# Kernel optimization log

Hardware: AMD Instinct MI355X
Metric: run time of the kernel (lower is better)

Reference implementation:

```python
import jax, jax.numpy as jnp
import numpy as np

B, D, O = 512, 256, 256
H = [512, 1024, 1024]

def _linear_params(key, fan_in, fan_out):
    kw, kb = jax.random.split(key)
    bound = 1.0 / np.sqrt(fan_in)
    W = jax.random.uniform(kw, (fan_out, fan_in), jnp.float32, -bound, bound)
    b = jax.random.uniform(kb, (fan_out,), jnp.float32, -bound, bound)
    return W, b

def setup_inputs() -> dict:
    key = jax.random.key(0)
    ks = jax.random.split(key, 7)
    input_values = jax.random.normal(ks[0], (B, D), jnp.float32)
    nan_flag = jax.random.uniform(ks[1], (B, D), jnp.float32)
    W_in, b_in = _linear_params(ks[2], D, H[0])          # input_layer: nan_flag_dim -> H[0]
    W_h1, b_h1 = _linear_params(ks[3], H[0], H[1])        # hidden layer 1
    W_h2, b_h2 = _linear_params(ks[4], H[1], H[2])        # hidden layer 2
    W_d, b_d = _linear_params(ks[5], H[2], D * O)         # output_branch_dense
    W_b, b_b = _linear_params(ks[6], H[2], O)             # output_branch_bias
    return {"input_values": input_values, "nan_flag": nan_flag, "training": False,
            "W_in": W_in, "b_in": b_in, "W_h1": W_h1, "b_h1": b_h1,
            "W_h2": W_h2, "b_h2": b_h2, "W_d": W_d, "b_d": b_d,
            "W_b": W_b, "b_b": b_b}

def reference(input_values, nan_flag, training, W_in, b_in, W_h1, b_h1, W_h2, b_h2, W_d, b_d, W_b, b_b):
    # training=False: dropout is identity, sample_missing branch skipped (default False)
    x = jax.nn.relu(nan_flag @ W_in.T + b_in)
    x = jax.nn.relu(x @ W_h1.T + b_h1)
    x = jax.nn.relu(x @ W_h2.T + b_h2)
    # per-sample compensation weights [B, D, O] and bias [B, O]
    comp_w = (x @ W_d.T + b_d).reshape(B, D, O)
    comp_b = x @ W_b.T + b_b
    # baddbmm: [B,1,D] @ [B,D,O] + [B,1,O] -> squeeze -> [B,O]
    out = comp_b + jnp.einsum('bd,bdo->bo', input_values, comp_w)
    return out
```

## Files before the change

kernel.cpp:

```cpp
#include <hip/hip_runtime.h>

#define B_  512
#define D_  256
#define O_  256
#define H2_ 1024

typedef __attribute__((ext_vector_type(4))) float  f32x4;
typedef __attribute__((ext_vector_type(8))) short  short8;
typedef __attribute__((ext_vector_type(4))) short  short4v;
typedef unsigned short ushort_t;

union S8u  { short4v v; unsigned u[2]; };
union S16u { short8  v; unsigned u[4]; };

__device__ __forceinline__ unsigned f32_bf16(float x) {
  unsigned u = __builtin_bit_cast(unsigned, x);
  return (u + 0x7fffu + ((u >> 16) & 1u)) >> 16;
}
__device__ __forceinline__ unsigned cvt_pk_bf16(float a, float b) {
  return f32_bf16(a) | (f32_bf16(b) << 16);
}

__device__ __forceinline__ void gload_lds16(const void* g, void* l) {
  __builtin_amdgcn_global_load_lds(
      (const __attribute__((address_space(1))) unsigned*)g,
      (__attribute__((address_space(3))) unsigned*)l, 16, 0, 0);
}

template <int RELU>
__global__ __launch_bounds__(256)
void gemm_bt64(const float* __restrict__ A, const float* __restrict__ Bm,
               const float* __restrict__ bias, float* __restrict__ C,
               int M, int N, int K) {
  __shared__ __align__(16) short As[64][72];
  __shared__ __align__(16) short Bs[64][72];
  const int t    = threadIdx.x;
  const int m0   = blockIdx.y * 64;
  const int n0   = blockIdx.x * 64;
  const int f4c  = t & 15;
  const int rg   = t >> 4;
  const int lane = t & 63;
  const int w    = t >> 6;
  const int wm   = (w & 1) * 32;
  const int wn   = (w >> 1) * 32;
  const int lr   = lane & 15;
  const int lq   = lane >> 4;

  f32x4 acc[2][2];
  #pragma unroll
  for (int i = 0; i < 2; ++i)
    #pragma unroll
    for (int j = 0; j < 2; ++j) acc[i][j] = f32x4{0.f, 0.f, 0.f, 0.f};

  for (int k0 = 0; k0 < K; k0 += 64) {
    #pragma unroll
    for (int j = 0; j < 4; ++j) {
      int r = rg + 16 * j;
      f32x4 av = *(const f32x4*)(A  + (size_t)(m0 + r) * K + k0 + f4c * 4);
      f32x4 bv = *(const f32x4*)(Bm + (size_t)(n0 + r) * K + k0 + f4c * 4);
      S8u sa; sa.u[0] = cvt_pk_bf16(av.x, av.y); sa.u[1] = cvt_pk_bf16(av.z, av.w);
      S8u sb; sb.u[0] = cvt_pk_bf16(bv.x, bv.y); sb.u[1] = cvt_pk_bf16(bv.z, bv.w);
      *(short4v*)&As[r][f4c * 4] = sa.v;
      *(short4v*)&Bs[r][f4c * 4] = sb.v;
    }
    __syncthreads();
    #pragma unroll
    for (int ks = 0; ks < 2; ++ks) {
      short8 a0 = *(const short8*)&As[wm + lr     ][ks * 32 + lq * 8];
      short8 a1 = *(const short8*)&As[wm + 16 + lr][ks * 32 + lq * 8];
      short8 b0 = *(const short8*)&Bs[wn + lr     ][ks * 32 + lq * 8];
      short8 b1 = *(const short8*)&Bs[wn + 16 + lr][ks * 32 + lq * 8];
      acc[0][0] = __builtin_amdgcn_mfma_f32_16x16x32_bf16(a0, b0, acc[0][0], 0, 0, 0);
      acc[0][1] = __builtin_amdgcn_mfma_f32_16x16x32_bf16(a0, b1, acc[0][1], 0, 0, 0);
      acc[1][0] = __builtin_amdgcn_mfma_f32_16x16x32_bf16(a1, b0, acc[1][0], 0, 0, 0);
      acc[1][1] = __builtin_amdgcn_mfma_f32_16x16x32_bf16(a1, b1, acc[1][1], 0, 0, 0);
    }
    __syncthreads();
  }
  #pragma unroll
  for (int mi = 0; mi < 2; ++mi)
    #pragma unroll
    for (int ni = 0; ni < 2; ++ni)
      #pragma unroll
      for (int r = 0; r < 4; ++r) {
        int row = m0 + wm + mi * 16 + lq * 4 + r;
        int col = n0 + wn + ni * 16 + lr;
        float v = acc[mi][ni][r] + bias[col];
        if (RELU) v = fmaxf(v, 0.f);
        C[(size_t)row * N + col] = v;
      }
}

__global__ __launch_bounds__(256)
void bias_d_kernel(const float* __restrict__ inp, const float* __restrict__ b_d,
                   float* __restrict__ out) {
  const int b = blockIdx.x;
  const int o = threadIdx.x;
  const float* ir = inp + (size_t)b * D_;
  float s = 0.f;
  for (int d = 0; d < D_; ++d)
    s += ir[d] * b_d[(size_t)d * O_ + o];
  out[(size_t)b * O_ + o] += s;
}

__global__ __launch_bounds__(256)
void cvt_f32_bf16(const float* __restrict__ in, ushort_t* __restrict__ out, int n8) {
  for (size_t i = (size_t)blockIdx.x * 256 + threadIdx.x; i < (size_t)n8;
       i += (size_t)gridDim.x * 256) {
    const float* p = in + i * 8;
    f32x4 v0 = *(const f32x4*)p;
    f32x4 v1 = *(const f32x4*)(p + 4);
    S16u s;
    s.u[0] = cvt_pk_bf16(v0.x, v0.y);
    s.u[1] = cvt_pk_bf16(v0.z, v0.w);
    s.u[2] = cvt_pk_bf16(v1.x, v1.y);
    s.u[3] = cvt_pk_bf16(v1.z, v1.w);
    *(short8*)(out + i * 8) = s.v;
  }
}

__global__ __launch_bounds__(512, 2)
void stage_b4(const ushort_t* __restrict__ x2b, const float* __restrict__ inp,
              const float* __restrict__ Wd, float* __restrict__ out) {
  __shared__ __align__(16) ushort_t As[2][256 * 32];
  __shared__ __align__(16) ushort_t Bs[2][256 * 32];
  const int t    = threadIdx.x;
  const int lin  = blockIdx.x + 8 * blockIdx.y;
  const int mt   = lin >> 8;
  const int nb   = lin & 255;
  const int d0   = (nb >> 4) * 16;
  const int og   = (nb & 15) * 16;
  const int bm   = mt * 256;
  const int lane = t & 63;
  const int w    = t >> 6;
  const int wm   = (w >> 1) * 64;
  const int wn   = (w & 1) * 128;
  const int lr   = lane & 15;
  const int lq   = lane >> 4;

  const int arow = lane >> 2;
  const int aswz = (lane & 3) ^ ((lane >> 3) & 3);
  const ushort_t* a_src0 = x2b + (size_t)(bm + (w & 3) * 0) * 0;
  const ushort_t* aptr[2];
  #pragma unroll
  for (int c = 0; c < 2; ++c)
    aptr[c] = x2b + (size_t)(bm + w * 32 + c * 16 + arow) * H2_ + aswz * 8;

  const int rr = t >> 1;
  const int hh = t & 1;
  const int wr = (d0 + (rr >> 4)) * 256 + og + (rr & 15);
  const float* bptr = Wd + (size_t)wr * H2_ + hh * 16;
  const int bsw = (rr >> 1) & 3;

  const int sl = (lq ^ ((lr >> 1) & 3)) * 8;

  f32x4 acc[4][8];
  #pragma unroll
  for (int mi = 0; mi < 4; ++mi)
    #pragma unroll
    for (int nj = 0; nj < 8; ++nj) acc[mi][nj] = f32x4{0.f, 0.f, 0.f, 0.f};

  f32x4 breg[4];

  auto stageA = [&](int k, int bf) {
    #pragma unroll
    for (int c = 0; c < 2; ++c)
      gload_lds16(aptr[c] + k * 32, &As[bf][(w * 32 + c * 16) * 32]);
  };
  auto loadB = [&](int k) {
    const float* p = bptr + k * 32;
    breg[0] = *(const f32x4*)p;
    breg[1] = *(const f32x4*)(p + 4);
    breg[2] = *(const f32x4*)(p + 8);
    breg[3] = *(const f32x4*)(p + 12);
  };
  auto writeB = [&](int bf) {
    S16u s0, s1;
    s0.u[0] = cvt_pk_bf16(breg[0].x, breg[0].y);
    s0.u[1] = cvt_pk_bf16(breg[0].z, breg[0].w);
    s0.u[2] = cvt_pk_bf16(breg[1].x, breg[1].y);
    s0.u[3] = cvt_pk_bf16(breg[1].z, breg[1].w);
    s1.u[0] = cvt_pk_bf16(breg[2].x, breg[2].y);
    s1.u[1] = cvt_pk_bf16(breg[2].z, breg[2].w);
    s1.u[2] = cvt_pk_bf16(breg[3].x, breg[3].y);
    s1.u[3] = cvt_pk_bf16(breg[3].z, breg[3].w);
    const int lcg0 = hh * 2;
    *(short8*)&Bs[bf][rr * 32 + (lcg0 ^ bsw) * 8]       = s0.v;
    *(short8*)&Bs[bf][rr * 32 + ((lcg0 + 1) ^ bsw) * 8] = s1.v;
  };

  stageA(0, 0);
  __builtin_amdgcn_sched_barrier(0);
  loadB(0);
  __builtin_amdgcn_sched_barrier(0);
  asm volatile("s_waitcnt vmcnt(0)" ::: "memory");
  writeB(0);
  loadB(1);
  __builtin_amdgcn_sched_barrier(0);
  asm volatile("s_waitcnt lgkmcnt(0)" ::: "memory");
  __builtin_amdgcn_s_barrier();

  int buf = 0;
  for (int k = 0; k < 32; ++k) {
    if (k < 31) {
      stageA(k + 1, buf ^ 1);
      __builtin_amdgcn_sched_barrier(0);
      asm volatile("s_waitcnt vmcnt(2)" ::: "memory");
      writeB(buf ^ 1);
    }
    if (k < 30) {
      loadB(k + 2);
      __builtin_amdgcn_sched_barrier(0);
    }

    short8 af[4], bf[8];
    #pragma unroll
    for (int mi = 0; mi < 4; ++mi)
      af[mi] = *(const short8*)&As[buf][(wm + mi * 16 + lr) * 32 + sl];
    #pragma unroll
    for (int nj = 0; nj < 8; ++nj)
      bf[nj] = *(const short8*)&Bs[buf][(wn + nj * 16 + lr) * 32 + sl];
    #pragma unroll
    for (int mi = 0; mi < 4; ++mi)
      #pragma unroll
      for (int nj = 0; nj < 8; ++nj)
        acc[mi][nj] = __builtin_amdgcn_mfma_f32_16x16x32_bf16(af[mi], bf[nj],
                                                              acc[mi][nj], 0, 0, 0);

    if (k < 31) {
      if (k < 30) { asm volatile("s_waitcnt vmcnt(4)" ::: "memory"); }
      else        { asm volatile("s_waitcnt vmcnt(0)" ::: "memory"); }
      asm volatile("s_waitcnt lgkmcnt(0)" ::: "memory");
      __builtin_amdgcn_s_barrier();
      buf ^= 1;
    }
  }

  const int dbase = d0 + (w & 1) * 8;
  const int o     = og + lr;
  #pragma unroll
  for (int mi = 0; mi < 4; ++mi)
    #pragma unroll
    for (int r = 0; r < 4; ++r) {
      const int row = bm + wm + mi * 16 + lq * 4 + r;
      f32x4 s0 = *(const f32x4*)(inp + (size_t)row * D_ + dbase);
      f32x4 s1 = *(const f32x4*)(inp + (size_t)row * D_ + dbase + 4);
      float v = s0.x * acc[mi][0][r] + s0.y * acc[mi][1][r] +
                s0.z * acc[mi][2][r] + s0.w * acc[mi][3][r] +
                s1.x * acc[mi][4][r] + s1.y * acc[mi][5][r] +
                s1.z * acc[mi][6][r] + s1.w * acc[mi][7][r];
      atomicAdd(out + (size_t)row * O_ + o, v);
    }
}

extern "C" void kernel_launch(void* const* d_in, const int* in_sizes, int n_in,
                              void* d_out, int out_size, void* d_ws, size_t ws_size,
                              hipStream_t stream) {
  const float* input = (const float*)d_in[0];
  const float* nanf  = (const float*)d_in[1];
  const float* W_in  = (const float*)d_in[3];
  const float* b_in  = (const float*)d_in[4];
  const float* W_h1  = (const float*)d_in[5];
  const float* b_h1  = (const float*)d_in[6];
  const float* W_h2  = (const float*)d_in[7];
  const float* b_h2  = (const float*)d_in[8];
  const float* W_d   = (const float*)d_in[9];
  const float* b_d   = (const float*)d_in[10];
  const float* W_b   = (const float*)d_in[11];
  const float* b_b   = (const float*)d_in[12];
  float* out = (float*)d_out;

  float* x0 = (float*)d_ws;
  float* x1 = x0 + 512 * 512;
  float* x2 = x1 + 512 * 1024;
  ushort_t* x2b = (ushort_t*)(x2 + 512 * 1024);

  gemm_bt64<1><<<dim3(512 / 64, 512 / 64), 256, 0, stream>>>(nanf, W_in, b_in, x0, 512, 512, 256);
  gemm_bt64<1><<<dim3(1024 / 64, 512 / 64), 256, 0, stream>>>(x0, W_h1, b_h1, x1, 512, 1024, 512);
  gemm_bt64<1><<<dim3(1024 / 64, 512 / 64), 256, 0, stream>>>(x1, W_h2, b_h2, x2, 512, 1024, 1024);
  cvt_f32_bf16<<<256, 256, 0, stream>>>(x2, x2b, 512 * 1024 / 8);
  gemm_bt64<0><<<dim3(256 / 64, 512 / 64), 256, 0, stream>>>(x2, W_b, b_b, out, 512, 256, 1024);
  bias_d_kernel<<<512, 256, 0, stream>>>(input, b_d, out);
  stage_b4<<<dim3(8, 64), 512, 0, stream>>>(x2b, input, W_d, out);
}
```

Baseline: 603.2 us.

## Shrink big GEMM tile to 128x128, fuse b_d bias, simplify B pipeline

Replaces the 256x256-tile, 512-thread stage_b4 kernel with a 128x128-tile, 256-thread stage_b5 that runs at 3 blocks per CU, with blocks ordered so that 4 M-tiles share each W_d slice. The separate bias_d_kernel launch is removed, and the b_d contribution is added inside the epilogue before scaling by the input values. The B prefetch is cut from two stages to one, with a full vmcnt(0) wait each iteration. Because the W_d tiles are now smaller, A and B are each reloaded more often relative to the compute. The shorter prefetch also hides less memory latency, traded against higher occupancy and one fewer launch.

New measurement: 584.1 us. 1.03x faster.

```diff
diff --git a/kernel.cpp b/kernel.cpp
--- a/kernel.cpp
+++ b/kernel.cpp
@@ -92,18 +92,6 @@
 }
 
 __global__ __launch_bounds__(256)
-void bias_d_kernel(const float* __restrict__ inp, const float* __restrict__ b_d,
-                   float* __restrict__ out) {
-  const int b = blockIdx.x;
-  const int o = threadIdx.x;
-  const float* ir = inp + (size_t)b * D_;
-  float s = 0.f;
-  for (int d = 0; d < D_; ++d)
-    s += ir[d] * b_d[(size_t)d * O_ + o];
-  out[(size_t)b * O_ + o] += s;
-}
-
-__global__ __launch_bounds__(256)
 void cvt_f32_bf16(const float* __restrict__ in, ushort_t* __restrict__ out, int n8) {
   for (size_t i = (size_t)blockIdx.x * 256 + threadIdx.x; i < (size_t)n8;
        i += (size_t)gridDim.x * 256) {
@@ -119,28 +107,29 @@
   }
 }
 
-__global__ __launch_bounds__(512, 2)
-void stage_b4(const ushort_t* __restrict__ x2b, const float* __restrict__ inp,
-              const float* __restrict__ Wd, float* __restrict__ out) {
-  __shared__ __align__(16) ushort_t As[2][256 * 32];
-  __shared__ __align__(16) ushort_t Bs[2][256 * 32];
+__global__ __launch_bounds__(256, 3)
+void stage_b5(const ushort_t* __restrict__ x2b, const float* __restrict__ inp,
+              const float* __restrict__ Wd, const float* __restrict__ bd,
+              float* __restrict__ out) {
+  __shared__ __align__(16) ushort_t As[2][128 * 32];
+  __shared__ __align__(16) ushort_t Bs[2][128 * 32];
   const int t    = threadIdx.x;
-  const int lin  = blockIdx.x + 8 * blockIdx.y;
-  const int mt   = lin >> 8;
-  const int nb   = lin & 255;
-  const int d0   = (nb >> 4) * 16;
+  const int x    = blockIdx.x;
+  const int q    = blockIdx.y;
+  const int mt   = q & 3;
+  const int nb   = (q >> 2) * 8 + x;
+  const int d0   = (nb >> 4) * 8;
   const int og   = (nb & 15) * 16;
-  const int bm   = mt * 256;
+  const int bm   = mt * 128;
   const int lane = t & 63;
   const int w    = t >> 6;
   const int wm   = (w >> 1) * 64;
-  const int wn   = (w & 1) * 128;
+  const int wn   = (w & 1) * 64;
   const int lr   = lane & 15;
   const int lq   = lane >> 4;
 
   const int arow = lane >> 2;
-  const int aswz = (lane & 3) ^ ((lane >> 3) & 3);
-  const ushort_t* a_src0 = x2b + (size_t)(bm + (w & 3) * 0) * 0;
+  const int aswz = (lane & 3) ^ ((arow >> 1) & 3);
   const ushort_t* aptr[2];
   #pragma unroll
   for (int c = 0; c < 2; ++c)
@@ -148,17 +137,17 @@
 
   const int rr = t >> 1;
   const int hh = t & 1;
-  const int wr = (d0 + (rr >> 4)) * 256 + og + (rr & 15);
+  const int wr = (d0 + (rr >> 4)) * O_ + og + (rr & 15);
   const float* bptr = Wd + (size_t)wr * H2_ + hh * 16;
   const int bsw = (rr >> 1) & 3;
 
   const int sl = (lq ^ ((lr >> 1) & 3)) * 8;
 
-  f32x4 acc[4][8];
+  f32x4 acc[4][4];
   #pragma unroll
   for (int mi = 0; mi < 4; ++mi)
     #pragma unroll
-    for (int nj = 0; nj < 8; ++nj) acc[mi][nj] = f32x4{0.f, 0.f, 0.f, 0.f};
+    for (int nj = 0; nj < 4; ++nj) acc[mi][nj] = f32x4{0.f, 0.f, 0.f, 0.f};
 
   f32x4 breg[4];
 
@@ -190,13 +179,9 @@
   };
 
   stageA(0, 0);
-  __builtin_amdgcn_sched_barrier(0);
   loadB(0);
-  __builtin_amdgcn_sched_barrier(0);
   asm volatile("s_waitcnt vmcnt(0)" ::: "memory");
   writeB(0);
-  loadB(1);
-  __builtin_amdgcn_sched_barrier(0);
   asm volatile("s_waitcnt lgkmcnt(0)" ::: "memory");
   __builtin_amdgcn_s_barrier();
 
@@ -204,51 +189,48 @@
   for (int k = 0; k < 32; ++k) {
     if (k < 31) {
       stageA(k + 1, buf ^ 1);
-      __builtin_amdgcn_sched_barrier(0);
-      asm volatile("s_waitcnt vmcnt(2)" ::: "memory");
-      writeB(buf ^ 1);
-    }
-    if (k < 30) {
-      loadB(k + 2);
-      __builtin_amdgcn_sched_barrier(0);
-    }
-
-    short8 af[4], bf[8];
+      loadB(k + 1);
+    }
+
+    short8 af[4], bfv[4];
     #pragma unroll
     for (int mi = 0; mi < 4; ++mi)
       af[mi] = *(const short8*)&As[buf][(wm + mi * 16 + lr) * 32 + sl];
     #pragma unroll
-    for (int nj = 0; nj < 8; ++nj)
-      bf[nj] = *(const short8*)&Bs[buf][(wn + nj * 16 + lr) * 32 + sl];
+    for (int nj = 0; nj < 4; ++nj)
+      bfv[nj] = *(const short8*)&Bs[buf][(wn + nj * 16 + lr) * 32 + sl];
     #pragma unroll
     for (int mi = 0; mi < 4; ++mi)
       #pragma unroll
-      for (int nj = 0; nj < 8; ++nj)
-        acc[mi][nj] = __builtin_amdgcn_mfma_f32_16x16x32_bf16(af[mi], bf[nj],
+      for (int nj = 0; nj < 4; ++nj)
+        acc[mi][nj] = __builtin_amdgcn_mfma_f32_16x16x32_bf16(af[mi], bfv[nj],
                                                               acc[mi][nj], 0, 0, 0);
 
     if (k < 31) {
-      if (k < 30) { asm volatile("s_waitcnt vmcnt(4)" ::: "memory"); }
-      else        { asm volatile("s_waitcnt vmcnt(0)" ::: "memory"); }
+      asm volatile("s_waitcnt vmcnt(0)" ::: "memory");
+      writeB(buf ^ 1);
       asm volatile("s_waitcnt lgkmcnt(0)" ::: "memory");
       __builtin_amdgcn_s_barrier();
       buf ^= 1;
     }
   }
 
-  const int dbase = d0 + (w & 1) * 8;
+  const int dbase = d0 + (w & 1) * 4;
   const int o     = og + lr;
+  float bdv[4];
+  #pragma unroll
+  for (int nj = 0; nj < 4; ++nj)
+    bdv[nj] = bd[(size_t)(dbase + nj) * O_ + o];
   #pragma unroll
   for (int mi = 0; mi < 4; ++mi)
     #pragma unroll
     for (int r = 0; r < 4; ++r) {
       const int row = bm + wm + mi * 16 + lq * 4 + r;
-      f32x4 s0 = *(const f32x4*)(inp + (size_t)row * D_ + dbase);
-      f32x4 s1 = *(const f32x4*)(inp + (size_t)row * D_ + dbase + 4);
-      float v = s0.x * acc[mi][0][r] + s0.y * acc[mi][1][r] +
-                s0.z * acc[mi][2][r] + s0.w * acc[mi][3][r] +
-                s1.x * acc[mi][4][r] + s1.y * acc[mi][5][r] +
-                s1.z * acc[mi][6][r] + s1.w * acc[mi][7][r];
+      f32x4 sc = *(const f32x4*)(inp + (size_t)row * D_ + dbase);
+      float v = sc.x * (acc[mi][0][r] + bdv[0]) +
+                sc.y * (acc[mi][1][r] + bdv[1]) +
+                sc.z * (acc[mi][2][r] + bdv[2]) +
+                sc.w * (acc[mi][3][r] + bdv[3]);
       atomicAdd(out + (size_t)row * O_ + o, v);
     }
 }
@@ -280,6 +262,5 @@
   gemm_bt64<1><<<dim3(1024 / 64, 512 / 64), 256, 0, stream>>>(x1, W_h2, b_h2, x2, 512, 1024, 1024);
   cvt_f32_bf16<<<256, 256, 0, stream>>>(x2, x2b, 512 * 1024 / 8);
   gemm_bt64<0><<<dim3(256 / 64, 512 / 64), 256, 0, stream>>>(x2, W_b, b_b, out, 512, 256, 1024);
-  bias_d_kernel<<<512, 256, 0, stream>>>(input, b_d, out);
-  stage_b4<<<dim3(8, 64), 512, 0, stream>>>(x2b, input, W_d, out);
-}
+  stage_b5<<<dim3(8, 256), 256, 0, stream>>>(x2b, input, W_d, b_d, out);
+}
```
